# Performance work log

Hardware: AMD Instinct MI355X
Metric: run time of the kernel (lower is better)

## Reference

```python
import jax, jax.numpy as jnp
import numpy as np


def _maxpool2x2(x):
    # x: [B, C, H, W] -> [B, C, H//2, W//2], 2x2 max pool stride 2
    B, C, H, W = x.shape
    return x.reshape(B, C, H // 2, 2, W // 2, 2).max(axis=(3, 5))


def _conv1x1(w, x):
    # w: [O, I], x: [B, I, H, W] -> [B, O, H, W]
    return jnp.einsum('oi,bihw->bohw', w, x)


def setup_inputs() -> dict:
    key = jax.random.key(0)
    ks = jax.random.split(key, 5)
    B, C, H, W = 16, 64, 64, 64
    c8, c2 = C // 8, C // 2
    x = jax.random.normal(ks[0], (B, C, H, W), dtype=jnp.float32)
    # 1x1 conv weights (spectral_norm is a training-time weight reparameterization;
    # here we use the effective weights directly, scaled for stability)
    w_theta = jax.random.normal(ks[1], (c8, C), dtype=jnp.float32) / np.sqrt(C)
    w_phi = jax.random.normal(ks[2], (c8, C), dtype=jnp.float32) / np.sqrt(C)
    w_g = jax.random.normal(ks[3], (c2, C), dtype=jnp.float32) / np.sqrt(C)
    w_o = jax.random.normal(ks[4], (C, c2), dtype=jnp.float32) / np.sqrt(c2)
    gamma = jnp.ones((1,), dtype=jnp.float32)
    return {"x": x, "w_theta": w_theta, "w_phi": w_phi, "w_g": w_g, "w_o": w_o, "gamma": gamma}


def reference(x, w_theta, w_phi, w_g, w_o, gamma):
    B, C, H, W = x.shape
    c8, c2 = C // 8, C // 2
    hw, hw4 = H * W, (H * W) // 4
    theta = _conv1x1(w_theta, x).reshape(B, c8, hw)            # [B, c8, hw]
    phi = _maxpool2x2(_conv1x1(w_phi, x)).reshape(B, c8, hw4)   # [B, c8, hw/4]
    attn = jax.nn.softmax(jnp.einsum('bcq,bck->bqk', theta, phi), axis=-1)  # [B, hw, hw/4]
    g = _maxpool2x2(_conv1x1(w_g, x)).reshape(B, c2, hw4)       # [B, c2, hw/4]
    attn_g = jnp.einsum('bck,bqk->bcq', g, attn).reshape(B, c2, H, W)
    out = x + gamma * _conv1x1(w_o, attn_g)
    return out
```

## Files before the change

kernel.cpp:

```cpp
#include <hip/hip_runtime.h>
#include <hip/hip_bf16.h>

#define B_  16
#define C_  64
#define HW  4096
#define KP  1024
#define LOG2E 1.44269504088896f

typedef short short8 __attribute__((ext_vector_type(8)));
typedef float floatx16 __attribute__((ext_vector_type(16)));

union Frag { uint4 u; short8 s; };

#define G_ROW      2064
#define ATTN_ROW   144
#define UNION_SZ   73728
#define WO_OFF     UNION_SZ
#define WO_ROW     80
#define L_OFF      (WO_OFF + 5120)
#define LDS_BYTES  (L_OFF + 2048)

__device__ __forceinline__ unsigned cvt_pk_bf16(float lo, float hi) {
    unsigned r;
    asm("v_cvt_pk_bf16_f32 %0, %1, %2" : "=v"(r) : "v"(lo), "v"(hi));
    return r;
}
#define PLSWAP(a, b) asm("v_permlane32_swap_b32 %0, %1" : "+v"(a), "+v"(b))

__device__ __forceinline__ void build_pfrags(const float* p, Frag& f0, Frag& f1) {
    unsigned u0 = cvt_pk_bf16(p[0], p[1]);
    unsigned u1 = cvt_pk_bf16(p[2], p[3]);
    unsigned u2 = cvt_pk_bf16(p[4], p[5]);
    unsigned u3 = cvt_pk_bf16(p[6], p[7]);
    PLSWAP(u0, u2);
    PLSWAP(u1, u3);
    f0.u.x = u0; f0.u.y = u1; f0.u.z = u2; f0.u.w = u3;
    unsigned v0 = cvt_pk_bf16(p[8],  p[9]);
    unsigned v1 = cvt_pk_bf16(p[10], p[11]);
    unsigned v2 = cvt_pk_bf16(p[12], p[13]);
    unsigned v3 = cvt_pk_bf16(p[14], p[15]);
    PLSWAP(v0, v2);
    PLSWAP(v1, v3);
    f1.u.x = v0; f1.u.y = v1; f1.u.z = v2; f1.u.w = v3;
}

__global__ __launch_bounds__(256) void convpool_kernel(
    const float* __restrict__ x,
    const float* __restrict__ w_theta,
    const float* __restrict__ w_phi,
    const float* __restrict__ w_g,
    __hip_bfloat16* __restrict__ theta16,
    __hip_bfloat16* __restrict__ phi16,
    __hip_bfloat16* __restrict__ gT)
{
    __shared__ float conv[48 * 257];
    const int bi = blockIdx.x;
    const int b  = bi >> 4;
    const int rg = bi & 15;
    const int t  = threadIdx.x;
    const int q  = rg * 256 + t;

    const float* xb = x + (size_t)b * C_ * HW + q;

    float xv[64];
    #pragma unroll
    for (int c = 0; c < C_; ++c) xv[c] = xb[(size_t)c * HW];
    unsigned r[32];
    #pragma unroll
    for (int i = 0; i < 32; ++i) r[i] = cvt_pk_bf16(xv[2 * i], xv[2 * i + 1]);

    const int lane = t & 63;
    const int ln   = lane & 31;
    const int hi   = lane >> 5;
    const int wv   = t >> 6;

    const float* wrow0 = (ln < 8)  ? (w_theta + ln * C_)
                       : (ln < 16) ? (w_phi + (ln - 8) * C_)
                                   : (w_g + (ln - 16) * C_);
    const float* wrow1 = (ln < 16) ? (w_g + (16 + ln) * C_) : (w_g + 31 * C_);

    Frag B0[4], B1[4];
    #pragma unroll
    for (int k = 0; k < 4; ++k) {
        const float* p0 = wrow0 + 16 * k + 8 * hi;
        const float4 f0 = *(const float4*)(p0);
        const float4 f1 = *(const float4*)(p0 + 4);
        B0[k].u.x = cvt_pk_bf16(f0.x, f0.y); B0[k].u.y = cvt_pk_bf16(f0.z, f0.w);
        B0[k].u.z = cvt_pk_bf16(f1.x, f1.y); B0[k].u.w = cvt_pk_bf16(f1.z, f1.w);
        const float* p1 = wrow1 + 16 * k + 8 * hi;
        const float4 g0 = *(const float4*)(p1);
        const float4 g1 = *(const float4*)(p1 + 4);
        B1[k].u.x = cvt_pk_bf16(g0.x, g0.y); B1[k].u.y = cvt_pk_bf16(g0.z, g0.w);
        B1[k].u.z = cvt_pk_bf16(g1.x, g1.y); B1[k].u.w = cvt_pk_bf16(g1.z, g1.w);
    }

    floatx16 D00 = {}, D01 = {}, D10 = {}, D11 = {};
    #pragma unroll
    for (int k = 0; k < 4; ++k) {
        unsigned a0 = r[8*k+0], a1 = r[8*k+1], a2 = r[8*k+2], a3 = r[8*k+3];
        unsigned b0 = r[8*k+4], b1 = r[8*k+5], b2 = r[8*k+6], b3 = r[8*k+7];
        PLSWAP(a0, b0); PLSWAP(a1, b1); PLSWAP(a2, b2); PLSWAP(a3, b3);
        Frag loF, hiF;
        loF.u.x = a0; loF.u.y = a1; loF.u.z = a2; loF.u.w = a3;
        hiF.u.x = b0; hiF.u.y = b1; hiF.u.z = b2; hiF.u.w = b3;
        D00 = __builtin_amdgcn_mfma_f32_32x32x16_bf16(loF.s, B0[k].s, D00, 0, 0, 0);
        D01 = __builtin_amdgcn_mfma_f32_32x32x16_bf16(loF.s, B1[k].s, D01, 0, 0, 0);
        D10 = __builtin_amdgcn_mfma_f32_32x32x16_bf16(hiF.s, B0[k].s, D10, 0, 0, 0);
        D11 = __builtin_amdgcn_mfma_f32_32x32x16_bf16(hiF.s, B1[k].s, D11, 0, 0, 0);
    }

    #pragma unroll
    for (int rI = 0; rI < 16; ++rI) {
        const int row = (rI & 3) + 8 * (rI >> 2) + 4 * hi;
        conv[ln * 257 + (wv * 64 + row)]      = D00[rI];
        conv[ln * 257 + (wv * 64 + 32 + row)] = D10[rI];
        if (ln < 16) {
            conv[(32 + ln) * 257 + (wv * 64 + row)]      = D01[rI];
            conv[(32 + ln) * 257 + (wv * 64 + 32 + row)] = D11[rI];
        }
    }
    __syncthreads();

    {
        float th[8];
        #pragma unroll
        for (int oc = 0; oc < 8; ++oc) th[oc] = conv[oc * 257 + t] * LOG2E;
        uint4 u, z = {0u, 0u, 0u, 0u};
        u.x = cvt_pk_bf16(th[0], th[1]);
        u.y = cvt_pk_bf16(th[2], th[3]);
        u.z = cvt_pk_bf16(th[4], th[5]);
        u.w = cvt_pk_bf16(th[6], th[7]);
        __hip_bfloat16* tp = theta16 + ((size_t)b * HW + q) * 16;
        *(uint4*)(tp)     = u;
        *(uint4*)(tp + 8) = z;
    }

    for (int wi = t; wi < 40 * 64; wi += 256) {
        const int oc = (wi >> 6) + 8;
        const int kl = wi & 63;
        const int pr = kl >> 5, pc = kl & 31;
        const int i00 = pr * 128 + pc * 2;
        const float* cp = conv + oc * 257;
        const float v = fmaxf(fmaxf(cp[i00], cp[i00 + 1]),
                              fmaxf(cp[i00 + 64], cp[i00 + 65]));
        const int kg = (2 * rg + pr) * 32 + pc;
        if (oc < 16) phi16[((size_t)b * KP + kg) * 16 + (oc - 8)] = __float2bfloat16(v);
        else         gT[((size_t)b * 32 + (oc - 16)) * KP + kg]   = __float2bfloat16(v);
    }
    {
        uint4 z = {0u, 0u, 0u, 0u};
        for (int wi = t; wi < 64; wi += 256) {
            const int kg = 2 * rg * 32 + wi;
            *(uint4*)(phi16 + ((size_t)b * KP + kg) * 16 + 8) = z;
        }
    }
}

__global__ __launch_bounds__(512, 2) void attn_kernel(
    const float* __restrict__ x,
    const float* __restrict__ w_o,
    const float* __restrict__ gamma_p,
    const __hip_bfloat16* __restrict__ theta16,
    const __hip_bfloat16* __restrict__ phi16,
    const __hip_bfloat16* __restrict__ gT,
    float* __restrict__ out)
{
    __shared__ __align__(16) char lds[LDS_BYTES];
    const int t = threadIdx.x;
    const int bid = (blockIdx.x & 7) * 32 + (blockIdx.x >> 3);
    const int b   = bid >> 4;
    const int qb0 = (bid & 15) * 256;

    {
        const uint4* src = (const uint4*)(gT + (size_t)b * 32 * KP);
        #pragma unroll
        for (int i = 0; i < 8; ++i) {
            const int gi = t + 512 * i;
            const int c = gi >> 7, kk = gi & 127;
            *(uint4*)(lds + c * G_ROW + kk * 16) = src[gi];
        }
    }
    if (t < 256) {
        const int co = t >> 2, part = t & 3;
        const float4* wsrc = (const float4*)(w_o + co * 32 + part * 8);
        const float4 f0 = wsrc[0], f1 = wsrc[1];
        uint4 u;
        u.x = cvt_pk_bf16(f0.x, f0.y); u.y = cvt_pk_bf16(f0.z, f0.w);
        u.z = cvt_pk_bf16(f1.x, f1.y); u.w = cvt_pk_bf16(f1.z, f1.w);
        *(uint4*)(lds + WO_OFF + co * WO_ROW + part * 16) = u;
    }
    __syncthreads();

    const int lane = t & 63;
    const int wv   = t >> 6;
    const int h    = wv >> 2;
    const int qp   = wv & 3;
    const int hi   = lane >> 5;
    const int ln   = lane & 31;
    const int qt0  = qp * 64, qt1 = qt0 + 32;
    const int kbase = h * 512;

    const uint4* thb = (const uint4*)(theta16 + ((size_t)b * HW + qb0) * 16);
    Frag bth0, bth1;
    bth0.u = thb[(qt0 + ln) * 2 + hi];
    bth1.u = thb[(qt1 + ln) * 2 + hi];

    const uint4* phb = (const uint4*)(phi16 + ((size_t)b * KP + kbase) * 16);
    const char*  gp  = lds + ln * G_ROW + kbase * 2 + hi * 16;

    floatx16 czero = {};
    floatx16 O0 = {}, O1 = {};
    float l0 = 0.f, l1 = 0.f;

    #pragma unroll 2
    for (int kb = 0; kb < 16; ++kb) {
        Frag aphi, gf0, gf1;
        aphi.u = phb[(kb * 32 + ln) * 2 + hi];
        gf0.u  = *(const uint4*)(gp + kb * 64);
        gf1.u  = *(const uint4*)(gp + kb * 64 + 32);

        floatx16 S0 = __builtin_amdgcn_mfma_f32_32x32x16_bf16(aphi.s, bth0.s, czero, 0, 0, 0);
        floatx16 S1 = __builtin_amdgcn_mfma_f32_32x32x16_bf16(aphi.s, bth1.s, czero, 0, 0, 0);

        float p0[16], p1[16];
        float la = 0.f, lb = 0.f, lc = 0.f, ld = 0.f;
        #pragma unroll
        for (int rr = 0; rr < 16; rr += 2) {
            p0[rr]   = __builtin_amdgcn_exp2f(S0[rr]);   la += p0[rr];
            p0[rr+1] = __builtin_amdgcn_exp2f(S0[rr+1]); lb += p0[rr+1];
        }
        #pragma unroll
        for (int rr = 0; rr < 16; rr += 2) {
            p1[rr]   = __builtin_amdgcn_exp2f(S1[rr]);   lc += p1[rr];
            p1[rr+1] = __builtin_amdgcn_exp2f(S1[rr+1]); ld += p1[rr+1];
        }
        l0 += la + lb; l1 += lc + ld;

        Frag pa00, pa01, pa10, pa11;
        build_pfrags(p0, pa00, pa01);
        build_pfrags(p1, pa10, pa11);

        O0 = __builtin_amdgcn_mfma_f32_32x32x16_bf16(pa00.s, gf0.s, O0, 0, 0, 0);
        O0 = __builtin_amdgcn_mfma_f32_32x32x16_bf16(pa01.s, gf1.s, O0, 0, 0, 0);
        O1 = __builtin_amdgcn_mfma_f32_32x32x16_bf16(pa10.s, gf0.s, O1, 0, 0, 0);
        O1 = __builtin_amdgcn_mfma_f32_32x32x16_bf16(pa11.s, gf1.s, O1, 0, 0, 0);
    }

    __syncthreads();

    #pragma unroll
    for (int rr = 0; rr < 16; ++rr) {
        const int rm = (rr & 3) + 8 * (rr >> 2) + 4 * hi;
        *(float*)(lds + ((h << 8) + qt0 + rm) * ATTN_ROW + ln * 4) = O0[rr];
        *(float*)(lds + ((h << 8) + qt1 + rm) * ATTN_ROW + ln * 4) = O1[rr];
    }
    const float l0t = l0 + __shfl_xor(l0, 32, 64);
    const float l1t = l1 + __shfl_xor(l1, 32, 64);
    {
        const int   lq = hi ? (qt1 + ln) : (qt0 + ln);
        const float lw = hi ? l1t : l0t;
        *(float*)(lds + L_OFF + ((h << 8) + lq) * 4) = lw;
    }
    __syncthreads();

    const float gam = gamma_p[0];
    const int   qt  = wv * 32;
    const float lt  = *(const float*)(lds + L_OFF + (qt + ln) * 4)
                    + *(const float*)(lds + L_OFF + (256 + qt + ln) * 4);
    const float gl  = gam / lt;

    const char* ab0 = lds + (qt + ln) * ATTN_ROW + hi * 32;
    const char* ab1 = ab0 + 256 * ATTN_ROW;
    float4 a0 = *(const float4*)(ab0);
    float4 a1 = *(const float4*)(ab0 + 16);
    float4 a2 = *(const float4*)(ab0 + 64);
    float4 a3 = *(const float4*)(ab0 + 80);
    const float4 c0 = *(const float4*)(ab1);
    const float4 c1 = *(const float4*)(ab1 + 16);
    const float4 c2 = *(const float4*)(ab1 + 64);
    const float4 c3 = *(const float4*)(ab1 + 80);
    a0.x += c0.x; a0.y += c0.y; a0.z += c0.z; a0.w += c0.w;
    a1.x += c1.x; a1.y += c1.y; a1.z += c1.z; a1.w += c1.w;
    a2.x += c2.x; a2.y += c2.y; a2.z += c2.z; a2.w += c2.w;
    a3.x += c3.x; a3.y += c3.y; a3.z += c3.z; a3.w += c3.w;

    Frag bat0, bat1;
    bat0.u.x = cvt_pk_bf16(a0.x, a0.y); bat0.u.y = cvt_pk_bf16(a0.z, a0.w);
    bat0.u.z = cvt_pk_bf16(a1.x, a1.y); bat0.u.w = cvt_pk_bf16(a1.z, a1.w);
    bat1.u.x = cvt_pk_bf16(a2.x, a2.y); bat1.u.y = cvt_pk_bf16(a2.z, a2.w);
    bat1.u.z = cvt_pk_bf16(a3.x, a3.y); bat1.u.w = cvt_pk_bf16(a3.z, a3.w);

    const char* wb = lds + WO_OFF + ln * WO_ROW + hi * 16;
    Frag wa00, wa01, wa10, wa11;
    wa00.u = *(const uint4*)(wb);
    wa01.u = *(const uint4*)(wb + 32);
    wa10.u = *(const uint4*)(wb + 32 * WO_ROW);
    wa11.u = *(const uint4*)(wb + 32 * WO_ROW + 32);

    floatx16 D0 = __builtin_amdgcn_mfma_f32_32x32x16_bf16(wa00.s, bat0.s, czero, 0, 0, 0);
    D0 = __builtin_amdgcn_mfma_f32_32x32x16_bf16(wa01.s, bat1.s, D0, 0, 0, 0);
    floatx16 D1 = __builtin_amdgcn_mfma_f32_32x32x16_bf16(wa10.s, bat0.s, czero, 0, 0, 0);
    D1 = __builtin_amdgcn_mfma_f32_32x32x16_bf16(wa11.s, bat1.s, D1, 0, 0, 0);

    const int qg = qb0 + qt + ln;
    const float* xb = x   + (size_t)b * C_ * HW + qg;
    float*       ob = out + (size_t)b * C_ * HW + qg;
    #pragma unroll
    for (int rr = 0; rr < 16; ++rr) {
        const int co = (rr & 3) + 8 * (rr >> 2) + 4 * hi;
        ob[(size_t)co * HW]        = xb[(size_t)co * HW]        + gl * D0[rr];
        ob[(size_t)(co + 32) * HW] = xb[(size_t)(co + 32) * HW] + gl * D1[rr];
    }
}

extern "C" void kernel_launch(void* const* d_in, const int* in_sizes, int n_in,
                              void* d_out, int out_size, void* d_ws, size_t ws_size,
                              hipStream_t stream) {
    const float* x       = (const float*)d_in[0];
    const float* w_theta = (const float*)d_in[1];
    const float* w_phi   = (const float*)d_in[2];
    const float* w_g     = (const float*)d_in[3];
    const float* w_o     = (const float*)d_in[4];
    const float* gamma   = (const float*)d_in[5];
    float* out = (float*)d_out;

    __hip_bfloat16* theta16 = (__hip_bfloat16*)d_ws;
    __hip_bfloat16* phi16   = theta16 + (size_t)B_ * HW * 16;
    __hip_bfloat16* gT      = phi16   + (size_t)B_ * KP * 16;

    convpool_kernel<<<dim3(B_ * 16), dim3(256), 0, stream>>>(
        x, w_theta, w_phi, w_g, theta16, phi16, gT);
    attn_kernel<<<dim3(B_ * 16), dim3(512), 0, stream>>>(
        x, w_o, gamma, theta16, phi16, gT, out);
}
```

Before: 30.93 us.

## Split convpool into smaller blocks and stream x loads in chunks

The conv+pool kernel now launches twice as many blocks of 128 threads, each covering two image rows instead of four, which shrinks shared memory per block and spreads work over more CUs. The 64-element register array of x is replaced by two 16-float buffers that are double-buffered, so MFMA work on one chunk can overlap the loads for the next. This lowers register pressure and raises occupancy, at the cost of more blocks and more repeated weight-fragment loads.

```diff
diff --git a/kernel.cpp b/kernel.cpp
--- a/kernel.cpp
+++ b/kernel.cpp
@@ -44,7 +44,7 @@
     f1.u.x = v0; f1.u.y = v1; f1.u.z = v2; f1.u.w = v3;
 }
 
-__global__ __launch_bounds__(256) void convpool_kernel(
+__global__ __launch_bounds__(128) void convpool_kernel(
     const float* __restrict__ x,
     const float* __restrict__ w_theta,
     const float* __restrict__ w_phi,
@@ -53,21 +53,14 @@
     __hip_bfloat16* __restrict__ phi16,
     __hip_bfloat16* __restrict__ gT)
 {
-    __shared__ float conv[48 * 257];
+    __shared__ float conv[48 * 129];
     const int bi = blockIdx.x;
-    const int b  = bi >> 4;
-    const int rg = bi & 15;
+    const int b  = bi >> 5;
+    const int rg = bi & 31;
     const int t  = threadIdx.x;
-    const int q  = rg * 256 + t;
-
-    const float* xb = x + (size_t)b * C_ * HW + q;
-
-    float xv[64];
-    #pragma unroll
-    for (int c = 0; c < C_; ++c) xv[c] = xb[(size_t)c * HW];
-    unsigned r[32];
-    #pragma unroll
-    for (int i = 0; i < 32; ++i) r[i] = cvt_pk_bf16(xv[2 * i], xv[2 * i + 1]);
+    const int q  = rg * 128 + t;
+
+    const float* xp = x + (size_t)b * C_ * HW + q;
 
     const int lane = t & 63;
     const int ln   = lane & 31;
@@ -95,28 +88,50 @@
     }
 
     floatx16 D00 = {}, D01 = {}, D10 = {}, D11 = {};
-    #pragma unroll
-    for (int k = 0; k < 4; ++k) {
-        unsigned a0 = r[8*k+0], a1 = r[8*k+1], a2 = r[8*k+2], a3 = r[8*k+3];
-        unsigned b0 = r[8*k+4], b1 = r[8*k+5], b2 = r[8*k+6], b3 = r[8*k+7];
-        PLSWAP(a0, b0); PLSWAP(a1, b1); PLSWAP(a2, b2); PLSWAP(a3, b3);
-        Frag loF, hiF;
-        loF.u.x = a0; loF.u.y = a1; loF.u.z = a2; loF.u.w = a3;
-        hiF.u.x = b0; hiF.u.y = b1; hiF.u.z = b2; hiF.u.w = b3;
-        D00 = __builtin_amdgcn_mfma_f32_32x32x16_bf16(loF.s, B0[k].s, D00, 0, 0, 0);
-        D01 = __builtin_amdgcn_mfma_f32_32x32x16_bf16(loF.s, B1[k].s, D01, 0, 0, 0);
-        D10 = __builtin_amdgcn_mfma_f32_32x32x16_bf16(hiF.s, B0[k].s, D10, 0, 0, 0);
-        D11 = __builtin_amdgcn_mfma_f32_32x32x16_bf16(hiF.s, B1[k].s, D11, 0, 0, 0);
-    }
+
+#define CHUNK(BUF, KK)                                                          \
+    {                                                                           \
+        unsigned q0 = cvt_pk_bf16(BUF[0],  BUF[1]);                             \
+        unsigned q1 = cvt_pk_bf16(BUF[2],  BUF[3]);                             \
+        unsigned q2 = cvt_pk_bf16(BUF[4],  BUF[5]);                             \
+        unsigned q3 = cvt_pk_bf16(BUF[6],  BUF[7]);                             \
+        unsigned q4 = cvt_pk_bf16(BUF[8],  BUF[9]);                             \
+        unsigned q5 = cvt_pk_bf16(BUF[10], BUF[11]);                            \
+        unsigned q6 = cvt_pk_bf16(BUF[12], BUF[13]);                            \
+        unsigned q7 = cvt_pk_bf16(BUF[14], BUF[15]);                            \
+        PLSWAP(q0, q4); PLSWAP(q1, q5); PLSWAP(q2, q6); PLSWAP(q3, q7);         \
+        Frag loF, hiF;                                                          \
+        loF.u.x = q0; loF.u.y = q1; loF.u.z = q2; loF.u.w = q3;                 \
+        hiF.u.x = q4; hiF.u.y = q5; hiF.u.z = q6; hiF.u.w = q7;                 \
+        D00 = __builtin_amdgcn_mfma_f32_32x32x16_bf16(loF.s, B0[KK].s, D00, 0, 0, 0); \
+        D01 = __builtin_amdgcn_mfma_f32_32x32x16_bf16(loF.s, B1[KK].s, D01, 0, 0, 0); \
+        D10 = __builtin_amdgcn_mfma_f32_32x32x16_bf16(hiF.s, B0[KK].s, D10, 0, 0, 0); \
+        D11 = __builtin_amdgcn_mfma_f32_32x32x16_bf16(hiF.s, B1[KK].s, D11, 0, 0, 0); \
+    }
+
+    float xa[16], xc[16];
+    #pragma unroll
+    for (int c = 0; c < 16; ++c) xa[c] = xp[(size_t)c * HW];
+    #pragma unroll
+    for (int c = 0; c < 16; ++c) xc[c] = xp[(size_t)(16 + c) * HW];
+    CHUNK(xa, 0);
+    #pragma unroll
+    for (int c = 0; c < 16; ++c) xa[c] = xp[(size_t)(32 + c) * HW];
+    CHUNK(xc, 1);
+    #pragma unroll
+    for (int c = 0; c < 16; ++c) xc[c] = xp[(size_t)(48 + c) * HW];
+    CHUNK(xa, 2);
+    CHUNK(xc, 3);
+#undef CHUNK
 
     #pragma unroll
     for (int rI = 0; rI < 16; ++rI) {
         const int row = (rI & 3) + 8 * (rI >> 2) + 4 * hi;
-        conv[ln * 257 + (wv * 64 + row)]      = D00[rI];
-        conv[ln * 257 + (wv * 64 + 32 + row)] = D10[rI];
+        conv[ln * 129 + (wv * 64 + row)]      = D00[rI];
+        conv[ln * 129 + (wv * 64 + 32 + row)] = D10[rI];
         if (ln < 16) {
-            conv[(32 + ln) * 257 + (wv * 64 + row)]      = D01[rI];
-            conv[(32 + ln) * 257 + (wv * 64 + 32 + row)] = D11[rI];
+            conv[(32 + ln) * 129 + (wv * 64 + row)]      = D01[rI];
+            conv[(32 + ln) * 129 + (wv * 64 + 32 + row)] = D11[rI];
         }
     }
     __syncthreads();
@@ -124,7 +139,7 @@
     {
         float th[8];
         #pragma unroll
-        for (int oc = 0; oc < 8; ++oc) th[oc] = conv[oc * 257 + t] * LOG2E;
+        for (int oc = 0; oc < 8; ++oc) th[oc] = conv[oc * 129 + t] * LOG2E;
         uint4 u, z = {0u, 0u, 0u, 0u};
         u.x = cvt_pk_bf16(th[0], th[1]);
         u.y = cvt_pk_bf16(th[2], th[3]);
@@ -135,24 +150,20 @@
         *(uint4*)(tp + 8) = z;
     }
 
-    for (int wi = t; wi < 40 * 64; wi += 256) {
-        const int oc = (wi >> 6) + 8;
-        const int kl = wi & 63;
-        const int pr = kl >> 5, pc = kl & 31;
-        const int i00 = pr * 128 + pc * 2;
-        const float* cp = conv + oc * 257;
+    for (int wi = t; wi < 40 * 32; wi += 128) {
+        const int oc = (wi >> 5) + 8;
+        const int pc = wi & 31;
+        const int i00 = pc * 2;
+        const float* cp = conv + oc * 129;
         const float v = fmaxf(fmaxf(cp[i00], cp[i00 + 1]),
                               fmaxf(cp[i00 + 64], cp[i00 + 65]));
-        const int kg = (2 * rg + pr) * 32 + pc;
+        const int kg = rg * 32 + pc;
         if (oc < 16) phi16[((size_t)b * KP + kg) * 16 + (oc - 8)] = __float2bfloat16(v);
         else         gT[((size_t)b * 32 + (oc - 16)) * KP + kg]   = __float2bfloat16(v);
     }
-    {
+    if (t < 32) {
         uint4 z = {0u, 0u, 0u, 0u};
-        for (int wi = t; wi < 64; wi += 256) {
-            const int kg = 2 * rg * 32 + wi;
-            *(uint4*)(phi16 + ((size_t)b * KP + kg) * 16 + 8) = z;
-        }
+        *(uint4*)(phi16 + ((size_t)b * KP + rg * 32 + t) * 16 + 8) = z;
     }
 }
 
@@ -328,7 +339,7 @@
     __hip_bfloat16* phi16   = theta16 + (size_t)B_ * HW * 16;
     __hip_bfloat16* gT      = phi16   + (size_t)B_ * KP * 16;
 
-    convpool_kernel<<<dim3(B_ * 16), dim3(256), 0, stream>>>(
+    convpool_kernel<<<dim3(B_ * 32), dim3(128), 0, stream>>>(
         x, w_theta, w_phi, w_g, theta16, phi16, gT);
     attn_kernel<<<dim3(B_ * 16), dim3(512), 0, stream>>>(
         x, w_o, gamma, theta16, phi16, gT, out);
```

After: 31.45 us. No clear change (+1.7%).

## Fuse conv/pool and attention kernels with per-batch atomic barrier

Applied to the files above, without the earlier changes.

Merges the conv+pool kernel and the attention kernel into one launch. Each block stages its x tile in LDS, computes theta locally (kept in LDS instead of a global round trip) and writes pooled phi/g to global. It then waits on a per-batch atomic counter until all 16 blocks of that batch are done. The x tile is reused from LDS for the residual add instead of being reread from global. This adds a memset, a spin barrier that requires all 256 blocks to be co-resident, and large dynamic LDS use (about 155 KB per block).

```diff
diff --git a/kernel.cpp b/kernel.cpp
--- a/kernel.cpp
+++ b/kernel.cpp
@@ -12,13 +12,17 @@
 
 union Frag { uint4 u; short8 s; };
 
-#define G_ROW      2064
-#define ATTN_ROW   144
-#define UNION_SZ   73728
-#define WO_OFF     UNION_SZ
-#define WO_ROW     80
-#define L_OFF      (WO_OFF + 5120)
-#define LDS_BYTES  (L_OFF + 2048)
+#define X_OFF    0
+#define X_ROW    272
+#define TH_OFF   69632
+#define UN_OFF   77824
+#define CV_ROW   1028
+#define G_ROW    2064
+#define ATTN_ROW 144
+#define WO_OFF   151552
+#define WO_ROW   80
+#define L_OFF    156672
+#define LDS_BYTES 158720
 
 __device__ __forceinline__ unsigned cvt_pk_bf16(float lo, float hi) {
     unsigned r;
@@ -44,41 +48,52 @@
     f1.u.x = v0; f1.u.y = v1; f1.u.z = v2; f1.u.w = v3;
 }
 
-__global__ __launch_bounds__(256) void convpool_kernel(
+__global__ __launch_bounds__(512, 2) void fused_kernel(
     const float* __restrict__ x,
     const float* __restrict__ w_theta,
     const float* __restrict__ w_phi,
     const float* __restrict__ w_g,
-    __hip_bfloat16* __restrict__ theta16,
+    const float* __restrict__ w_o,
+    const float* __restrict__ gamma_p,
     __hip_bfloat16* __restrict__ phi16,
-    __hip_bfloat16* __restrict__ gT)
+    __hip_bfloat16* __restrict__ gT,
+    unsigned* __restrict__ cnt,
+    float* __restrict__ out)
 {
-    __shared__ float conv[48 * 257];
-    const int bi = blockIdx.x;
-    const int b  = bi >> 4;
-    const int rg = bi & 15;
-    const int t  = threadIdx.x;
-    const int q  = rg * 256 + t;
-
-    const float* xb = x + (size_t)b * C_ * HW + q;
-
-    float xv[64];
-    #pragma unroll
-    for (int c = 0; c < C_; ++c) xv[c] = xb[(size_t)c * HW];
-    unsigned r[32];
-    #pragma unroll
-    for (int i = 0; i < 32; ++i) r[i] = cvt_pk_bf16(xv[2 * i], xv[2 * i + 1]);
+    extern __shared__ __align__(16) char lds[];
+    const int t = threadIdx.x;
+    const int xcd = blockIdx.x & 7, slot = blockIdx.x >> 3;
+    const int b   = xcd * 2 + (slot >> 4);
+    const int qb  = slot & 15;
+    const int qb0 = qb * 256;
 
     const int lane = t & 63;
     const int ln   = lane & 31;
     const int hi   = lane >> 5;
     const int wv   = t >> 6;
 
+    {
+        const float* xs = x + (size_t)b * C_ * HW + qb0;
+        #pragma unroll
+        for (int i = 0; i < 32; ++i) {
+            const int idx = t + 512 * i;
+            const int c = idx >> 8, px = idx & 255;
+            *(float*)(lds + X_OFF + px * X_ROW + c * 4) = xs[(size_t)c * HW + px];
+        }
+    }
+    if (t < 256) {
+        const int co = t >> 2, part = t & 3;
+        const float4* wsrc = (const float4*)(w_o + co * 32 + part * 8);
+        const float4 f0 = wsrc[0], f1 = wsrc[1];
+        uint4 u;
+        u.x = cvt_pk_bf16(f0.x, f0.y); u.y = cvt_pk_bf16(f0.z, f0.w);
+        u.z = cvt_pk_bf16(f1.x, f1.y); u.w = cvt_pk_bf16(f1.z, f1.w);
+        *(uint4*)(lds + WO_OFF + co * WO_ROW + part * 16) = u;
+    }
     const float* wrow0 = (ln < 8)  ? (w_theta + ln * C_)
                        : (ln < 16) ? (w_phi + (ln - 8) * C_)
                                    : (w_g + (ln - 16) * C_);
     const float* wrow1 = (ln < 16) ? (w_g + (16 + ln) * C_) : (w_g + 31 * C_);
-
     Frag B0[4], B1[4];
     #pragma unroll
     for (int k = 0; k < 4; ++k) {
@@ -93,83 +108,67 @@
         B1[k].u.x = cvt_pk_bf16(g0.x, g0.y); B1[k].u.y = cvt_pk_bf16(g0.z, g0.w);
         B1[k].u.z = cvt_pk_bf16(g1.x, g1.y); B1[k].u.w = cvt_pk_bf16(g1.z, g1.w);
     }
-
-    floatx16 D00 = {}, D01 = {}, D10 = {}, D11 = {};
-    #pragma unroll
-    for (int k = 0; k < 4; ++k) {
-        unsigned a0 = r[8*k+0], a1 = r[8*k+1], a2 = r[8*k+2], a3 = r[8*k+3];
-        unsigned b0 = r[8*k+4], b1 = r[8*k+5], b2 = r[8*k+6], b3 = r[8*k+7];
-        PLSWAP(a0, b0); PLSWAP(a1, b1); PLSWAP(a2, b2); PLSWAP(a3, b3);
-        Frag loF, hiF;
-        loF.u.x = a0; loF.u.y = a1; loF.u.z = a2; loF.u.w = a3;
-        hiF.u.x = b0; hiF.u.y = b1; hiF.u.z = b2; hiF.u.w = b3;
-        D00 = __builtin_amdgcn_mfma_f32_32x32x16_bf16(loF.s, B0[k].s, D00, 0, 0, 0);
-        D01 = __builtin_amdgcn_mfma_f32_32x32x16_bf16(loF.s, B1[k].s, D01, 0, 0, 0);
-        D10 = __builtin_amdgcn_mfma_f32_32x32x16_bf16(hiF.s, B0[k].s, D10, 0, 0, 0);
-        D11 = __builtin_amdgcn_mfma_f32_32x32x16_bf16(hiF.s, B1[k].s, D11, 0, 0, 0);
-    }
-
-    #pragma unroll
-    for (int rI = 0; rI < 16; ++rI) {
-        const int row = (rI & 3) + 8 * (rI >> 2) + 4 * hi;
-        conv[ln * 257 + (wv * 64 + row)]      = D00[rI];
-        conv[ln * 257 + (wv * 64 + 32 + row)] = D10[rI];
-        if (ln < 16) {
-            conv[(32 + ln) * 257 + (wv * 64 + row)]      = D01[rI];
-            conv[(32 + ln) * 257 + (wv * 64 + 32 + row)] = D11[rI];
-        }
-    }
     __syncthreads();
 
     {
+        floatx16 D0 = {}, D1 = {};
+        const char* xr = lds + X_OFF + (wv * 32 + ln) * X_ROW;
+        #pragma unroll
+        for (int k = 0; k < 4; ++k) {
+            const float4 xf0 = *(const float4*)(xr + (16 * k + 8 * hi) * 4);
+            const float4 xf1 = *(const float4*)(xr + (16 * k + 8 * hi) * 4 + 16);
+            Frag a;
+            a.u.x = cvt_pk_bf16(xf0.x, xf0.y); a.u.y = cvt_pk_bf16(xf0.z, xf0.w);
+            a.u.z = cvt_pk_bf16(xf1.x, xf1.y); a.u.w = cvt_pk_bf16(xf1.z, xf1.w);
+            D0 = __builtin_amdgcn_mfma_f32_32x32x16_bf16(a.s, B0[k].s, D0, 0, 0, 0);
+            D1 = __builtin_amdgcn_mfma_f32_32x32x16_bf16(a.s, B1[k].s, D1, 0, 0, 0);
+        }
+        #pragma unroll
+        for (int r = 0; r < 16; ++r) {
+            const int px = wv * 32 + (r & 3) + 8 * (r >> 2) + 4 * hi;
+            *(float*)(lds + UN_OFF + ln * CV_ROW + px * 4) = D0[r];
+            if (ln < 16)
+                *(float*)(lds + UN_OFF + (32 + ln) * CV_ROW + px * 4) = D1[r];
+        }
+    }
+    __syncthreads();
+
+    if (t < 256) {
         float th[8];
         #pragma unroll
-        for (int oc = 0; oc < 8; ++oc) th[oc] = conv[oc * 257 + t] * LOG2E;
-        uint4 u, z = {0u, 0u, 0u, 0u};
-        u.x = cvt_pk_bf16(th[0], th[1]);
-        u.y = cvt_pk_bf16(th[2], th[3]);
-        u.z = cvt_pk_bf16(th[4], th[5]);
-        u.w = cvt_pk_bf16(th[6], th[7]);
-        __hip_bfloat16* tp = theta16 + ((size_t)b * HW + q) * 16;
-        *(uint4*)(tp)     = u;
-        *(uint4*)(tp + 8) = z;
-    }
-
-    for (int wi = t; wi < 40 * 64; wi += 256) {
+        for (int oc = 0; oc < 8; ++oc)
+            th[oc] = *(const float*)(lds + UN_OFF + oc * CV_ROW + t * 4) * LOG2E;
+        uint4 u; uint4 z = {0u, 0u, 0u, 0u};
+        u.x = cvt_pk_bf16(th[0], th[1]); u.y = cvt_pk_bf16(th[2], th[3]);
+        u.z = cvt_pk_bf16(th[4], th[5]); u.w = cvt_pk_bf16(th[6], th[7]);
+        *(uint4*)(lds + TH_OFF + t * 32)      = u;
+        *(uint4*)(lds + TH_OFF + t * 32 + 16) = z;
+    }
+    for (int wi = t; wi < 2560; wi += 512) {
         const int oc = (wi >> 6) + 8;
         const int kl = wi & 63;
         const int pr = kl >> 5, pc = kl & 31;
-        const int i00 = pr * 128 + pc * 2;
-        const float* cp = conv + oc * 257;
-        const float v = fmaxf(fmaxf(cp[i00], cp[i00 + 1]),
-                              fmaxf(cp[i00 + 64], cp[i00 + 65]));
-        const int kg = (2 * rg + pr) * 32 + pc;
+        const char* cp = lds + UN_OFF + oc * CV_ROW;
+        const int i0 = (pr * 128 + pc * 2) * 4;
+        const float v = fmaxf(fmaxf(*(const float*)(cp + i0),       *(const float*)(cp + i0 + 4)),
+                              fmaxf(*(const float*)(cp + i0 + 256), *(const float*)(cp + i0 + 260)));
+        const int kg = qb * 64 + pr * 32 + pc;
         if (oc < 16) phi16[((size_t)b * KP + kg) * 16 + (oc - 8)] = __float2bfloat16(v);
         else         gT[((size_t)b * 32 + (oc - 16)) * KP + kg]   = __float2bfloat16(v);
     }
-    {
+    if (t < 64) {
         uint4 z = {0u, 0u, 0u, 0u};
-        for (int wi = t; wi < 64; wi += 256) {
-            const int kg = 2 * rg * 32 + wi;
-            *(uint4*)(phi16 + ((size_t)b * KP + kg) * 16 + 8) = z;
-        }
-    }
-}
-
-__global__ __launch_bounds__(512, 2) void attn_kernel(
-    const float* __restrict__ x,
-    const float* __restrict__ w_o,
-    const float* __restrict__ gamma_p,
-    const __hip_bfloat16* __restrict__ theta16,
-    const __hip_bfloat16* __restrict__ phi16,
-    const __hip_bfloat16* __restrict__ gT,
-    float* __restrict__ out)
-{
-    __shared__ __align__(16) char lds[LDS_BYTES];
-    const int t = threadIdx.x;
-    const int bid = (blockIdx.x & 7) * 32 + (blockIdx.x >> 3);
-    const int b   = bid >> 4;
-    const int qb0 = (bid & 15) * 256;
+        *(uint4*)(phi16 + ((size_t)b * KP + qb * 64 + t) * 16 + 8) = z;
+    }
+
+    __syncthreads();
+    if (t == 0) {
+        __hip_atomic_fetch_add(cnt + b, 1u, __ATOMIC_RELEASE, __HIP_MEMORY_SCOPE_AGENT);
+        while (__hip_atomic_load(cnt + b, __ATOMIC_ACQUIRE, __HIP_MEMORY_SCOPE_AGENT) < 16u) {
+            __builtin_amdgcn_s_sleep(8);
+        }
+    }
+    __syncthreads();
 
     {
         const uint4* src = (const uint4*)(gT + (size_t)b * 32 * KP);
@@ -177,36 +176,22 @@
         for (int i = 0; i < 8; ++i) {
             const int gi = t + 512 * i;
             const int c = gi >> 7, kk = gi & 127;
-            *(uint4*)(lds + c * G_ROW + kk * 16) = src[gi];
-        }
-    }
-    if (t < 256) {
-        const int co = t >> 2, part = t & 3;
-        const float4* wsrc = (const float4*)(w_o + co * 32 + part * 8);
-        const float4 f0 = wsrc[0], f1 = wsrc[1];
-        uint4 u;
-        u.x = cvt_pk_bf16(f0.x, f0.y); u.y = cvt_pk_bf16(f0.z, f0.w);
-        u.z = cvt_pk_bf16(f1.x, f1.y); u.w = cvt_pk_bf16(f1.z, f1.w);
-        *(uint4*)(lds + WO_OFF + co * WO_ROW + part * 16) = u;
-    }
-    __syncthreads();
-
-    const int lane = t & 63;
-    const int wv   = t >> 6;
+            *(uint4*)(lds + UN_OFF + c * G_ROW + kk * 16) = src[gi];
+        }
+    }
+    __syncthreads();
+
     const int h    = wv >> 2;
     const int qp   = wv & 3;
-    const int hi   = lane >> 5;
-    const int ln   = lane & 31;
     const int qt0  = qp * 64, qt1 = qt0 + 32;
     const int kbase = h * 512;
 
-    const uint4* thb = (const uint4*)(theta16 + ((size_t)b * HW + qb0) * 16);
     Frag bth0, bth1;
-    bth0.u = thb[(qt0 + ln) * 2 + hi];
-    bth1.u = thb[(qt1 + ln) * 2 + hi];
+    bth0.u = *(const uint4*)(lds + TH_OFF + (qt0 + ln) * 32 + hi * 16);
+    bth1.u = *(const uint4*)(lds + TH_OFF + (qt1 + ln) * 32 + hi * 16);
 
     const uint4* phb = (const uint4*)(phi16 + ((size_t)b * KP + kbase) * 16);
-    const char*  gp  = lds + ln * G_ROW + kbase * 2 + hi * 16;
+    const char*  gp  = lds + UN_OFF + ln * G_ROW + kbase * 2 + hi * 16;
 
     floatx16 czero = {};
     floatx16 O0 = {}, O1 = {};
@@ -251,8 +236,8 @@
     #pragma unroll
     for (int rr = 0; rr < 16; ++rr) {
         const int rm = (rr & 3) + 8 * (rr >> 2) + 4 * hi;
-        *(float*)(lds + ((h << 8) + qt0 + rm) * ATTN_ROW + ln * 4) = O0[rr];
-        *(float*)(lds + ((h << 8) + qt1 + rm) * ATTN_ROW + ln * 4) = O1[rr];
+        *(float*)(lds + UN_OFF + ((h << 8) + qt0 + rm) * ATTN_ROW + ln * 4) = O0[rr];
+        *(float*)(lds + UN_OFF + ((h << 8) + qt1 + rm) * ATTN_ROW + ln * 4) = O1[rr];
     }
     const float l0t = l0 + __shfl_xor(l0, 32, 64);
     const float l1t = l1 + __shfl_xor(l1, 32, 64);
@@ -269,7 +254,7 @@
                     + *(const float*)(lds + L_OFF + (256 + qt + ln) * 4);
     const float gl  = gam / lt;
 
-    const char* ab0 = lds + (qt + ln) * ATTN_ROW + hi * 32;
+    const char* ab0 = lds + UN_OFF + (qt + ln) * ATTN_ROW + hi * 32;
     const char* ab1 = ab0 + 256 * ATTN_ROW;
     float4 a0 = *(const float4*)(ab0);
     float4 a1 = *(const float4*)(ab0 + 16);
@@ -303,13 +288,19 @@
     D1 = __builtin_amdgcn_mfma_f32_32x32x16_bf16(wa11.s, bat1.s, D1, 0, 0, 0);
 
     const int qg = qb0 + qt + ln;
-    const float* xb = x   + (size_t)b * C_ * HW + qg;
-    float*       ob = out + (size_t)b * C_ * HW + qg;
+    float* ob = out + (size_t)b * C_ * HW + qg;
+    const char* xr = lds + X_OFF + (qt + ln) * X_ROW;
     #pragma unroll
-    for (int rr = 0; rr < 16; ++rr) {
-        const int co = (rr & 3) + 8 * (rr >> 2) + 4 * hi;
-        ob[(size_t)co * HW]        = xb[(size_t)co * HW]        + gl * D0[rr];
-        ob[(size_t)(co + 32) * HW] = xb[(size_t)(co + 32) * HW] + gl * D1[rr];
+    for (int g4 = 0; g4 < 4; ++g4) {
+        const float4 xa = *(const float4*)(xr + (g4 * 8 + 4 * hi) * 4);
+        const float4 xb = *(const float4*)(xr + (g4 * 8 + 4 * hi + 32) * 4);
+        #pragma unroll
+        for (int j = 0; j < 4; ++j) {
+            const int rI = 4 * g4 + j;
+            const int co = j + 8 * g4 + 4 * hi;
+            ob[(size_t)co * HW]        = ((const float*)&xa)[j] + gl * D0[rI];
+            ob[(size_t)(co + 32) * HW] = ((const float*)&xb)[j] + gl * D1[rI];
+        }
     }
 }
 
@@ -324,12 +315,13 @@
     const float* gamma   = (const float*)d_in[5];
     float* out = (float*)d_out;
 
-    __hip_bfloat16* theta16 = (__hip_bfloat16*)d_ws;
-    __hip_bfloat16* phi16   = theta16 + (size_t)B_ * HW * 16;
-    __hip_bfloat16* gT      = phi16   + (size_t)B_ * KP * 16;
-
-    convpool_kernel<<<dim3(B_ * 16), dim3(256), 0, stream>>>(
-        x, w_theta, w_phi, w_g, theta16, phi16, gT);
-    attn_kernel<<<dim3(B_ * 16), dim3(512), 0, stream>>>(
-        x, w_o, gamma, theta16, phi16, gT, out);
+    __hip_bfloat16* phi16 = (__hip_bfloat16*)d_ws;
+    __hip_bfloat16* gT    = phi16 + (size_t)B_ * KP * 16;
+    unsigned* cnt = (unsigned*)((char*)d_ws + 1572864);
+
+    hipMemsetAsync(cnt, 0, 16 * sizeof(unsigned), stream);
+    hipFuncSetAttribute((const void*)fused_kernel,
+                        hipFuncAttributeMaxDynamicSharedMemorySize, LDS_BYTES);
+    fused_kernel<<<dim3(256), dim3(512), LDS_BYTES, stream>>>(
+        x, w_theta, w_phi, w_g, w_o, gamma, phi16, gT, cnt, out);
 }
```

Result: slower. 42.26 us (+36.6%).
